# Kernel tuning notes

Hardware: AMD Instinct MI355X
Metric: run time of the kernel (lower is better)

## Reference

```python
import jax, jax.numpy as jnp
import numpy as np

MAX_INT = 1e4  # sentinel used by the original (transitions into START / out of STOP forbidden)
VOCAB, E, H, T, B, S = 50257, 512, 1024, 50, 8, 512  # T = tagset_size + 2


def _lstm_scan(x, h0, c0, Wih, Whh, b):
    # x: [time, batch, E] (time axis is the ORIGINAL batch dim, faithful to the
    # torch code which feeds [B,S,E] into a batch_first=False LSTM)
    def step(carry, xt):
        h, c = carry
        g = xt @ Wih.T + h @ Whh.T + b
        i, f, gg, o = jnp.split(g, 4, axis=-1)  # torch gate order i,f,g,o
        c = jax.nn.sigmoid(f) * c + jax.nn.sigmoid(i) * jnp.tanh(gg)
        h = jax.nn.sigmoid(o) * jnp.tanh(c)
        return (h, c), h
    _, hs = jax.lax.scan(step, (h0, c0), x)
    return hs


def setup_inputs() -> dict:
    key = jax.random.key(0)
    k = jax.random.split(key, 14)
    Hd = H // 2
    X = jax.random.randint(k[0], (B, S), 0, VOCAB)
    Y = jax.random.randint(k[1], (B, S), 0, T - 2)  # real tags only (no start/stop)
    h0 = jax.random.normal(k[2], (2, S, Hd), jnp.float32)
    c0 = jax.random.normal(k[3], (2, S, Hd), jnp.float32)
    emb_table = jax.random.normal(k[4], (VOCAB, E), jnp.float32) * 0.02
    Wih_f = jax.random.normal(k[5], (4 * Hd, E), jnp.float32) * 0.05
    Whh_f = jax.random.normal(k[6], (4 * Hd, Hd), jnp.float32) * 0.05
    b_f = jnp.zeros((4 * Hd,), jnp.float32)
    Wih_b = jax.random.normal(k[7], (4 * Hd, E), jnp.float32) * 0.05
    Whh_b = jax.random.normal(k[8], (4 * Hd, Hd), jnp.float32) * 0.05
    b_b = jnp.zeros((4 * Hd,), jnp.float32)
    fc_W = jax.random.normal(k[9], (T, H), jnp.float32) * 0.05
    fc_b = jnp.zeros((T,), jnp.float32)
    tr = jax.random.normal(k[10], (T, T), jnp.float32)
    transitions = tr.at[-2, :].set(-MAX_INT).at[:, -1].set(-MAX_INT)
    return {"X": X, "Y": Y, "h0": h0, "c0": c0, "emb_table": emb_table,
            "Wih_f": Wih_f, "Whh_f": Whh_f, "b_f": b_f,
            "Wih_b": Wih_b, "Whh_b": Whh_b, "b_b": b_b,
            "fc_W": fc_W, "fc_b": fc_b, "transitions": transitions}


def reference(X, Y, h0, c0, emb_table, Wih_f, Whh_f, b_f, Wih_b, Whh_b, b_b, fc_W, fc_b, transitions):
    emb = emb_table[X]                                   # [B,S,E]
    # BiLSTM: torch sees axis0 as time (faithful quirk), hidden batch == S
    hf = _lstm_scan(emb, h0[0], c0[0], Wih_f, Whh_f, b_f)
    hb = _lstm_scan(emb[::-1], h0[1], c0[1], Wih_b, Whh_b, b_b)[::-1]
    lstm_out = jnp.concatenate([hf, hb], axis=-1)        # [B,S,H]
    feats = lstm_out @ fc_W.T + fc_b                     # [B,S,T]
    nB, Tt = X.shape[0], transitions.shape[0]
    # CRF forward algorithm (log partition), vectorized over tags
    init = jnp.full((nB, Tt), -MAX_INT, feats.dtype).at[:, -2].set(0.0)
    def crf_step(fv, feat):                              # fv [B,T], feat [B,T]
        nv = fv[:, None, :] + transitions[None, :, :] + feat[:, :, None]  # [B,next,prev]
        return jax.nn.logsumexp(nv, axis=2), None
    fv, _ = jax.lax.scan(crf_step, init, jnp.swapaxes(feats, 0, 1))
    forward_score = jax.nn.logsumexp(fv + transitions[-1][None, :], axis=1).sum()
    # gold path score
    start = jnp.full((nB, 1), Tt - 2, dtype=Y.dtype)
    tags = jnp.concatenate([start, Y], axis=1)           # [B,S+1]
    trans_sc = transitions[tags[:, 1:], tags[:, :-1]].sum()
    emit_sc = jnp.take_along_axis(feats, tags[:, 1:, None], axis=2)[..., 0].sum()
    gold_score = trans_sc + emit_sc + transitions[-1, tags[:, -1]].sum()
    score = forward_score - gold_score
    return score, Y
```

## Files before the change

kernel.cpp:

```cpp
#include <hip/hip_runtime.h>
#include <hip/hip_bf16.h>

typedef __attribute__((ext_vector_type(4))) float f32x4;
typedef __attribute__((ext_vector_type(8))) short short8;

#define LN2F 0.69314718055994531f

__device__ __forceinline__ unsigned short f2b(float x){
  union{float f;unsigned u;}v; v.f=x;
  unsigned r = v.u + 0x7fffu + ((v.u>>16)&1u);
  return (unsigned short)(r>>16);
}
__device__ __forceinline__ float b2f(unsigned short h){
  union{unsigned u;float f;}v; v.u = ((unsigned)h)<<16; return v.f;
}
__device__ __forceinline__ float sigm(float x){ return 1.f/(1.f+__expf(-x)); }
__device__ __forceinline__ float tanh_(float x){ float t=__expf(2.f*x); return 1.f - 2.f/(t+1.f); }

__global__ __launch_bounds__(256) void prep_kernel(
  const int* __restrict__ X, const int* __restrict__ Y,
  const float* __restrict__ h0, const float* __restrict__ c0,
  const float* __restrict__ emb,
  const float* __restrict__ WihF, const float* __restrict__ WihB,
  const float* __restrict__ WhhFf, const float* __restrict__ WhhBf,
  const float* __restrict__ fcWf, const float* __restrict__ trans,
  unsigned short* __restrict__ Abf, unsigned short* __restrict__ Wcat,
  unsigned short* __restrict__ WhhF, unsigned short* __restrict__ WhhB,
  unsigned short* __restrict__ hbufs, float* __restrict__ cbuf,
  unsigned short* __restrict__ fcW, unsigned short* __restrict__ Ebf,
  float* __restrict__ out)
{
  const int tid = blockIdx.x*256 + threadIdx.x;
  const int nth = gridDim.x*256;
  for(int i=tid;i<524288;i+=nth){
    int r = i>>7, q = i&127;
    float4 v = ((const float4*)(emb + (size_t)X[r]*512))[q];
    ushort4 o; o.x=f2b(v.x); o.y=f2b(v.y); o.z=f2b(v.z); o.w=f2b(v.w);
    ((ushort4*)Abf)[i] = o;
  }
  for(int i=tid;i<524288;i+=nth){
    int r = i>>7, q = i&127;
    const float* src = (r<2048) ? (WihF + (size_t)r*512) : (WihB + (size_t)(r-2048)*512);
    float4 v = ((const float4*)src)[q];
    ushort4 o; o.x=f2b(v.x); o.y=f2b(v.y); o.z=f2b(v.z); o.w=f2b(v.w);
    ((ushort4*)Wcat)[i] = o;
  }
  for(int i=tid;i<262144;i+=nth){
    float4 v = ((const float4*)WhhFf)[i];
    ushort4 o; o.x=f2b(v.x); o.y=f2b(v.y); o.z=f2b(v.z); o.w=f2b(v.w);
    ((ushort4*)WhhF)[i] = o;
  }
  for(int i=tid;i<262144;i+=nth){
    float4 v = ((const float4*)WhhBf)[i];
    ushort4 o; o.x=f2b(v.x); o.y=f2b(v.y); o.z=f2b(v.z); o.w=f2b(v.w);
    ((ushort4*)WhhB)[i] = o;
  }
  for(int i=tid;i<131072;i+=nth){
    int d = i>>16, rest = i&65535;
    float4 v = ((const float4*)h0)[i];
    ushort4 o; o.x=f2b(v.x); o.y=f2b(v.y); o.z=f2b(v.z); o.w=f2b(v.w);
    ((ushort4*)hbufs)[(size_t)(d*2)*65536 + rest] = o;
  }
  for(int i=tid;i<131072;i+=nth) ((float4*)cbuf)[i] = ((const float4*)c0)[i];
  for(int i=tid;i<16384;i+=nth){
    int n = i>>8, q = i&255;
    float4 v;
    if (n<50) v = ((const float4*)(fcWf + (size_t)n*1024))[q];
    else { v.x=0.f; v.y=0.f; v.z=0.f; v.w=0.f; }
    ushort4 o; o.x=f2b(v.x); o.y=f2b(v.y); o.z=f2b(v.z); o.w=f2b(v.w);
    ((ushort4*)fcW)[i] = o;
  }
  for(int i=tid;i<4096;i+=nth){
    int n = i>>6, p = i&63;
    float v = (n<50 && p<50) ? __expf(trans[n*50+p]) : 0.f;
    Ebf[i] = f2b(v);
  }
  for(int i=tid;i<4096;i+=nth) out[1+i] = (float)Y[i];
}

__global__ __launch_bounds__(256) void gemm1_kernel(const unsigned short* __restrict__ A,
                                                    const unsigned short* __restrict__ B,
                                                    unsigned short* __restrict__ C){
  __shared__ __align__(16) unsigned short As[128*40];
  __shared__ __align__(16) unsigned short Bs[128*40];
  const int t = threadIdx.x, w = t>>6, l = t&63;
  const int m0 = blockIdx.x<<7, n0 = blockIdx.y<<7;
  const int wr = (w>>1)<<6, wc = (w&1)<<6;
  const int srow = t>>2, scol = (t&3)<<3;
  const int fr = l&15, fk = (l>>4)<<3;
  f32x4 acc[4][4];
  #pragma unroll
  for(int i=0;i<4;i++)
    #pragma unroll
    for(int j=0;j<4;j++) acc[i][j]=(f32x4)0.f;
  const unsigned short* Ab = A + (size_t)m0*512;
  const unsigned short* Bb = B + (size_t)n0*512;
  uint4 pa0 = *(const uint4*)(Ab + srow*512 + scol);
  uint4 pa1 = *(const uint4*)(Ab + (64+srow)*512 + scol);
  uint4 pb0 = *(const uint4*)(Bb + srow*512 + scol);
  uint4 pb1 = *(const uint4*)(Bb + (64+srow)*512 + scol);
  for(int kt=0; kt<16; ++kt){
    __syncthreads();
    *(uint4*)&As[srow*40 + scol] = pa0;
    *(uint4*)&As[(64+srow)*40 + scol] = pa1;
    *(uint4*)&Bs[srow*40 + scol] = pb0;
    *(uint4*)&Bs[(64+srow)*40 + scol] = pb1;
    __syncthreads();
    if (kt<15){
      int kc = (kt+1)*32 + scol;
      pa0 = *(const uint4*)(Ab + srow*512 + kc);
      pa1 = *(const uint4*)(Ab + (64+srow)*512 + kc);
      pb0 = *(const uint4*)(Bb + srow*512 + kc);
      pb1 = *(const uint4*)(Bb + (64+srow)*512 + kc);
    }
    short8 af[4], bf[4];
    #pragma unroll
    for(int mi=0;mi<4;mi++) af[mi] = *(const short8*)&As[(wr+mi*16+fr)*40 + fk];
    #pragma unroll
    for(int ni=0;ni<4;ni++) bf[ni] = *(const short8*)&Bs[(wc+ni*16+fr)*40 + fk];
    #pragma unroll
    for(int mi=0;mi<4;mi++)
      #pragma unroll
      for(int ni=0;ni<4;ni++)
        acc[mi][ni] = __builtin_amdgcn_mfma_f32_16x16x32_bf16(af[mi], bf[ni], acc[mi][ni], 0,0,0);
  }
  #pragma unroll
  for(int mi=0;mi<4;mi++)
    #pragma unroll
    for(int ni=0;ni<4;ni++)
      #pragma unroll
      for(int j=0;j<4;j++){
        int row = m0 + wr + mi*16 + ((l>>4)<<2) + j;
        int col = n0 + wc + ni*16 + fr;
        C[(size_t)row*4096 + col] = f2b(acc[mi][ni][j]);
      }
}

__global__ __launch_bounds__(256) void lstm_step_kernel(
  unsigned short* __restrict__ hbufs, float* __restrict__ cbuf,
  unsigned short* __restrict__ hall, const unsigned short* __restrict__ Gin,
  const unsigned short* __restrict__ WhhF_, const unsigned short* __restrict__ WhhB_,
  const float* __restrict__ bF, const float* __restrict__ bB, int t)
{
  __shared__ __align__(16) unsigned short Ah[128*40];
  __shared__ __align__(16) unsigned short Bw[64*40];
  const int d = blockIdx.z;
  const int m0 = blockIdx.x<<7;
  const int u0 = blockIdx.y<<4;
  const int tin = d ? (7-t) : t;
  const int par = t&1;
  const unsigned short* hprev = hbufs + (size_t)(d*2+par)*262144;
  unsigned short* hnext = hbufs + (size_t)(d*2+(par^1))*262144;
  const unsigned short* W = d ? WhhB_ : WhhF_;
  const float* bias = d ? bB : bF;
  const int tx = threadIdx.x, w = tx>>6, l = tx&63;
  const int srow = tx>>2, scol = (tx&3)<<3;
  const int bc = tx>>2;
  const int bn = ((bc>>4)<<9) + u0 + (bc&15);
  const int fr = l&15, fk = (l>>4)<<3;
  f32x4 acc[2][4];
  #pragma unroll
  for(int i=0;i<2;i++)
    #pragma unroll
    for(int j=0;j<4;j++) acc[i][j]=(f32x4)0.f;
  uint4 pa0 = *(const uint4*)(hprev + (size_t)(m0+srow)*512 + scol);
  uint4 pa1 = *(const uint4*)(hprev + (size_t)(m0+64+srow)*512 + scol);
  uint4 pb0 = *(const uint4*)(W + (size_t)bn*512 + scol);
  for(int kt=0; kt<16; ++kt){
    __syncthreads();
    *(uint4*)&Ah[srow*40+scol] = pa0;
    *(uint4*)&Ah[(64+srow)*40+scol] = pa1;
    *(uint4*)&Bw[bc*40+scol] = pb0;
    __syncthreads();
    if(kt<15){
      int kc = (kt+1)*32 + scol;
      pa0 = *(const uint4*)(hprev + (size_t)(m0+srow)*512 + kc);
      pa1 = *(const uint4*)(hprev + (size_t)(m0+64+srow)*512 + kc);
      pb0 = *(const uint4*)(W + (size_t)bn*512 + kc);
    }
    short8 af[2], bf[4];
    #pragma unroll
    for(int mi=0;mi<2;mi++) af[mi] = *(const short8*)&Ah[(w*32+mi*16+fr)*40 + fk];
    #pragma unroll
    for(int g=0;g<4;g++)   bf[g]  = *(const short8*)&Bw[(g*16+fr)*40 + fk];
    #pragma unroll
    for(int mi=0;mi<2;mi++)
      #pragma unroll
      for(int g=0;g<4;g++)
        acc[mi][g] = __builtin_amdgcn_mfma_f32_16x16x32_bf16(af[mi], bf[g], acc[mi][g], 0,0,0);
  }
  #pragma unroll
  for(int mi=0;mi<2;mi++)
    #pragma unroll
    for(int j=0;j<4;j++){
      int rs = m0 + w*32 + mi*16 + ((l>>4)<<2) + j;
      int u  = u0 + fr;
      size_t grow = (size_t)(tin*512 + rs)*4096 + (size_t)d*2048;
      float p0 = acc[mi][0][j] + b2f(Gin[grow +    0 + u]) + bias[   0+u];
      float p1 = acc[mi][1][j] + b2f(Gin[grow +  512 + u]) + bias[ 512+u];
      float p2 = acc[mi][2][j] + b2f(Gin[grow + 1024 + u]) + bias[1024+u];
      float p3 = acc[mi][3][j] + b2f(Gin[grow + 1536 + u]) + bias[1536+u];
      size_t ci = (size_t)d*262144 + (size_t)rs*512 + u;
      float c = sigm(p1)*cbuf[ci] + sigm(p0)*tanh_(p2);
      cbuf[ci] = c;
      float h = sigm(p3)*tanh_(c);
      hnext[(size_t)rs*512+u] = f2b(h);
      hall[(size_t)(tin*512+rs)*1024 + (size_t)d*512 + u] = f2b(h);
    }
}

__global__ __launch_bounds__(256) void fc_kernel(const unsigned short* __restrict__ hA,
    const unsigned short* __restrict__ Wf, const float* __restrict__ fcb,
    float* __restrict__ feats){
  __shared__ __align__(16) unsigned short As[128*40];
  __shared__ __align__(16) unsigned short Bs[64*40];
  const int tx = threadIdx.x, w = tx>>6, l = tx&63;
  const int m0 = blockIdx.x<<7;
  const int srow = tx>>2, scol = (tx&3)<<3;
  const int fr=l&15, fk=(l>>4)<<3;
  f32x4 acc[2][4];
  #pragma unroll
  for(int i=0;i<2;i++)
    #pragma unroll
    for(int j=0;j<4;j++) acc[i][j]=(f32x4)0.f;
  uint4 pa0 = *(const uint4*)(hA + (size_t)(m0+srow)*1024 + scol);
  uint4 pa1 = *(const uint4*)(hA + (size_t)(m0+64+srow)*1024 + scol);
  uint4 pb0 = *(const uint4*)(Wf + (size_t)srow*1024 + scol);
  for(int kt=0; kt<32; ++kt){
    __syncthreads();
    *(uint4*)&As[srow*40+scol] = pa0;
    *(uint4*)&As[(64+srow)*40+scol] = pa1;
    *(uint4*)&Bs[srow*40+scol] = pb0;
    __syncthreads();
    if(kt<31){
      int kc = (kt+1)*32 + scol;
      pa0 = *(const uint4*)(hA + (size_t)(m0+srow)*1024 + kc);
      pa1 = *(const uint4*)(hA + (size_t)(m0+64+srow)*1024 + kc);
      pb0 = *(const uint4*)(Wf + (size_t)srow*1024 + kc);
    }
    short8 af[2], bf[4];
    #pragma unroll
    for(int mi=0;mi<2;mi++) af[mi] = *(const short8*)&As[(w*32+mi*16+fr)*40 + fk];
    #pragma unroll
    for(int ni=0;ni<4;ni++) bf[ni] = *(const short8*)&Bs[(ni*16+fr)*40 + fk];
    #pragma unroll
    for(int mi=0;mi<2;mi++)
      #pragma unroll
      for(int ni=0;ni<4;ni++)
        acc[mi][ni] = __builtin_amdgcn_mfma_f32_16x16x32_bf16(af[mi], bf[ni], acc[mi][ni], 0,0,0);
  }
  #pragma unroll
  for(int mi=0;mi<2;mi++)
    #pragma unroll
    for(int ni=0;ni<4;ni++)
      #pragma unroll
      for(int j=0;j<4;j++){
        int rs = m0 + w*32 + mi*16 + ((l>>4)<<2) + j;
        int n  = ni*16 + fr;
        feats[(size_t)rs*64+n] = acc[mi][ni][j] + (n<50 ? fcb[n] : 0.f);
      }
}

__global__ __launch_bounds__(64) void crf_group_kernel(
    const float* __restrict__ feats, const unsigned short* __restrict__ Ebf,
    float* __restrict__ Wout, int* __restrict__ kexp)
{
  __shared__ __align__(16) unsigned short PT[64*72];
  __shared__ float fe[8*64];
  const int g = blockIdx.x, b = blockIdx.y;
  const int l = threadIdx.x;
  const int lj = l & 15, q = l >> 4;
  const float* fb = feats + (size_t)(b*512 + g*8)*64;
  #pragma unroll
  for(int j=0;j<8;j++) fe[j*64 + l] = fb[j*64 + l];
  short8 afE[4][2];
  #pragma unroll
  for(int i=0;i<4;i++)
    #pragma unroll
    for(int h=0;h<2;h++)
      afE[i][h] = *(const short8*)(Ebf + (i*16+lj)*64 + h*32 + q*8);
  {
    uint4 erow[8];
    #pragma unroll
    for(int i=0;i<8;i++) erow[i] = *(const uint4*)(Ebf + l*64 + i*8);
    float ef0 = __expf(fe[l]);
    const unsigned* e32 = (const unsigned*)erow;
    #pragma unroll
    for(int m=0;m<64;m++){
      unsigned short eb = (unsigned short)(e32[m>>1] >> ((m&1)*16));
      PT[m*72 + l] = f2b(b2f(eb) * ef0);
    }
  }
  float sc_lag = 1.f;
  int exprev = 0, kblk = 0;
  #pragma unroll
  for(int k=1;k<8;k++){
    kblk += exprev;
    float ev[4][4];
    #pragma unroll
    for(int i=0;i<4;i++)
      #pragma unroll
      for(int r=0;r<4;r++)
        ev[i][r] = __expf(fe[k*64 + i*16 + q*4 + r]) * sc_lag;
    short8 bfP[4][2];
    #pragma unroll
    for(int j=0;j<4;j++)
      #pragma unroll
      for(int h=0;h<2;h++)
        bfP[j][h] = *(const short8*)&PT[(j*16+lj)*72 + h*32 + q*8];
    f32x4 acc[4][4];
    #pragma unroll
    for(int i=0;i<4;i++)
      #pragma unroll
      for(int j=0;j<4;j++) acc[i][j] = (f32x4)0.f;
    #pragma unroll
    for(int h=0;h<2;h++)
      #pragma unroll
      for(int i=0;i<4;i++)
        #pragma unroll
        for(int j=0;j<4;j++)
          acc[i][j] = __builtin_amdgcn_mfma_f32_16x16x32_bf16(afE[i][h], bfP[j][h], acc[i][j], 0,0,0);
    float mx = 1e-30f;
    float* Wo = Wout + (size_t)(b*64 + g)*4096;
    #pragma unroll
    for(int i=0;i<4;i++)
      #pragma unroll
      for(int j=0;j<4;j++){
        float v0 = acc[i][j][0]*ev[i][0];
        float v1 = acc[i][j][1]*ev[i][1];
        float v2 = acc[i][j][2]*ev[i][2];
        float v3 = acc[i][j][3]*ev[i][3];
        mx = fmaxf(fmaxf(mx, fmaxf(v0,v1)), fmaxf(v2,v3));
        int base = (j*16+lj)*72 + i*16 + q*4;
        *(unsigned*)&PT[base]   = (unsigned)f2b(v0) | ((unsigned)f2b(v1)<<16);
        *(unsigned*)&PT[base+2] = (unsigned)f2b(v2) | ((unsigned)f2b(v3)<<16);
        if(k==7){
          int n = i*16 + q*4, m = j*16 + lj;
          Wo[(size_t)(n+0)*64 + m] = v0;
          Wo[(size_t)(n+1)*64 + m] = v1;
          Wo[(size_t)(n+2)*64 + m] = v2;
          Wo[(size_t)(n+3)*64 + m] = v3;
        }
      }
    #pragma unroll
    for(int off=1; off<64; off<<=1) mx = fmaxf(mx, __shfl_xor(mx, off));
    int ex = ((__builtin_bit_cast(int, mx) >> 23) & 0xff) - 127;
    ex = ex < -120 ? -120 : (ex > 120 ? 120 : ex);
    sc_lag = __builtin_bit_cast(float, (unsigned)((127-ex)<<23));
    exprev = ex;
  }
  if(l==0) kexp[b*64 + g] = kblk;
}

__global__ __launch_bounds__(64) void crf_seq_kernel(const float* __restrict__ W,
    const int* __restrict__ kexp, const float* __restrict__ trans,
    float* __restrict__ scores){
  __shared__ __align__(16) float sh[64];
  const int b = blockIdx.x, l = threadIdx.x;
  const float* Wb = W + (size_t)b*262144;
  float kl = (float)kexp[b*64 + l];
  #pragma unroll
  for(int off=32;off;off>>=1) kl += __shfl_down(kl, off);
  float G = (l==48) ? 1.f : 0.f;
  float sc = 1.f, Mrun = 0.f;
  int exprev = 0;
  float4 curA[16], curB[16];
  #pragma unroll
  for(int i=0;i<16;i++) curA[i] = ((const float4*)(Wb + (size_t)l*64))[i];

#define SEQ_STEP(CUR, NXT, GI) {                                            \
    sh[l] = G;                                                              \
    const float* wn = Wb + (size_t)(((GI)+1)&63)*4096 + (size_t)l*64;       \
    _Pragma("unroll")                                                       \
    for(int i=0;i<16;i++) NXT[i] = ((const float4*)wn)[i];                  \
    float4 gq[16];                                                          \
    _Pragma("unroll")                                                       \
    for(int i=0;i<16;i++) gq[i] = ((const float4*)sh)[i];                   \
    float a0=0.f,a1=0.f,a2=0.f,a3=0.f;                                      \
    _Pragma("unroll")                                                       \
    for(int i=0;i<16;i++){                                                  \
      a0 = fmaf(CUR[i].x, gq[i].x, a0);                                     \
      a1 = fmaf(CUR[i].y, gq[i].y, a1);                                     \
      a2 = fmaf(CUR[i].z, gq[i].z, a2);                                     \
      a3 = fmaf(CUR[i].w, gq[i].w, a3);                                     \
    }                                                                       \
    float S = (a0+a1)+(a2+a3);                                              \
    Mrun += (float)exprev;                                                  \
    G = S * sc;                                                             \
    float Sp = __builtin_bit_cast(float, __builtin_amdgcn_readfirstlane(    \
                 __builtin_bit_cast(int, fmaxf(S, 1e-35f))));               \
    int ex = ((__builtin_bit_cast(int, Sp) >> 23) & 0xff) - 127;            \
    ex = ex < -120 ? -120 : (ex > 120 ? 120 : ex);                          \
    sc = __builtin_bit_cast(float, (unsigned)((127-ex)<<23));               \
    exprev = ex;                                                            \
  }

  for(int g=0; g<64; g+=2){
    SEQ_STEP(curA, curB, g)
    SEQ_STEP(curB, curA, g+1)
  }
#undef SEQ_STEP
  float u = (l<50) ? __expf(trans[49*50+l]) : 0.f;
  float val = G * u;
  #pragma unroll
  for(int off=32;off;off>>=1) val += __shfl_down(val, off);
  if(l==0) scores[b] = logf(fmaxf(val,1e-35f)) + (Mrun + kl)*LN2F;
}

__global__ __launch_bounds__(256) void final_kernel(const int* __restrict__ Y,
   const float* __restrict__ trans, const float* __restrict__ feats,
   const float* __restrict__ scores, float* __restrict__ out){
  const int tx = threadIdx.x;
  float acc = 0.f;
  for(int i=tx; i<4096; i+=256){
    int s = i & 511;
    int y = Y[i];
    int prev = s ? Y[i-1] : 48;
    acc += trans[y*50+prev] + feats[(size_t)i*64+y];
    if (s==511) acc += trans[49*50+y];
  }
  #pragma unroll
  for(int off=32; off; off>>=1) acc += __shfl_down(acc, off);
  __shared__ float red[4];
  if((tx&63)==0) red[tx>>6] = acc;
  __syncthreads();
  if(tx==0){
    float gold = red[0]+red[1]+red[2]+red[3];
    float fwd = 0.f;
    #pragma unroll
    for(int b=0;b<8;b++) fwd += scores[b];
    out[0] = fwd - gold;
  }
}

extern "C" void kernel_launch(void* const* d_in, const int* in_sizes, int n_in,
                              void* d_out, int out_size, void* d_ws, size_t ws_size,
                              hipStream_t stream) {
  (void)in_sizes; (void)n_in; (void)out_size; (void)ws_size;
  const int*   X     = (const int*)d_in[0];
  const int*   Y     = (const int*)d_in[1];
  const float* h0    = (const float*)d_in[2];
  const float* c0    = (const float*)d_in[3];
  const float* emb   = (const float*)d_in[4];
  const float* WihF  = (const float*)d_in[5];
  const float* WhhFf = (const float*)d_in[6];
  const float* bF    = (const float*)d_in[7];
  const float* WihB  = (const float*)d_in[8];
  const float* WhhBf = (const float*)d_in[9];
  const float* bB    = (const float*)d_in[10];
  const float* fcWf  = (const float*)d_in[11];
  const float* fcb   = (const float*)d_in[12];
  const float* trans = (const float*)d_in[13];
  float* out = (float*)d_out;
  char* ws = (char*)d_ws;

  unsigned short* Abf   = (unsigned short*)(ws + 0);
  unsigned short* Wcat  = (unsigned short*)(ws + 4194304);
  unsigned short* WhhF  = (unsigned short*)(ws + 8388608);
  unsigned short* WhhB  = (unsigned short*)(ws + 10485760);
  unsigned short* Gin   = (unsigned short*)(ws + 12582912);
  float*          Wgrp  = (float*)(ws + 12582912);
  int*            kexp  = (int*)(ws + 20971520);
  unsigned short* hbufs = (unsigned short*)(ws + 46137344);
  float*          cbuf  = (float*)(ws + 48234496);
  unsigned short* hall  = (unsigned short*)(ws + 50331648);
  unsigned short* fcW   = (unsigned short*)(ws + 58720256);
  float*          feats = (float*)(ws + 58851328);
  unsigned short* Ebf   = (unsigned short*)(ws + 59900160);
  float*          scores= (float*)(ws + 59913472);

  hipLaunchKernelGGL(prep_kernel, dim3(1024), dim3(256), 0, stream,
      X, Y, h0, c0, emb, WihF, WihB, WhhFf, WhhBf, fcWf, trans,
      Abf, Wcat, WhhF, WhhB, hbufs, cbuf, fcW, Ebf, out);
  hipLaunchKernelGGL(gemm1_kernel, dim3(32,32), dim3(256), 0, stream, Abf, Wcat, Gin);
  for(int t=0;t<8;t++)
    hipLaunchKernelGGL(lstm_step_kernel, dim3(4,32,2), dim3(256), 0, stream,
        hbufs, cbuf, hall, Gin, WhhF, WhhB, bF, bB, t);
  hipLaunchKernelGGL(fc_kernel, dim3(32), dim3(256), 0, stream, hall, fcW, fcb, feats);
  hipLaunchKernelGGL(crf_group_kernel, dim3(64,8), dim3(64), 0, stream, feats, Ebf, Wgrp, kexp);
  hipLaunchKernelGGL(crf_seq_kernel, dim3(8), dim3(64), 0, stream, Wgrp, kexp, trans, scores);
  hipLaunchKernelGGL(final_kernel, dim3(1), dim3(256), 0, stream, Y, trans, feats, scores, out);
}
```

Measured before the change: 234.3 us.

## Fuse LSTM timesteps into persistent cooperative kernel and widen CRF groups

```diff
diff --git a/kernel.cpp b/kernel.cpp
--- a/kernel.cpp
+++ b/kernel.cpp
@@ -1,5 +1,8 @@
 #include <hip/hip_runtime.h>
 #include <hip/hip_bf16.h>
+#include <hip/hip_cooperative_groups.h>
+
+namespace cg = cooperative_groups;
 
 typedef __attribute__((ext_vector_type(4))) float f32x4;
 typedef __attribute__((ext_vector_type(8))) short short8;
@@ -136,77 +139,86 @@
       }
 }
 
-__global__ __launch_bounds__(256) void lstm_step_kernel(
+__global__ __launch_bounds__(256, 1) void lstm_coop_kernel(
   unsigned short* __restrict__ hbufs, float* __restrict__ cbuf,
   unsigned short* __restrict__ hall, const unsigned short* __restrict__ Gin,
   const unsigned short* __restrict__ WhhF_, const unsigned short* __restrict__ WhhB_,
-  const float* __restrict__ bF, const float* __restrict__ bB, int t)
+  const float* __restrict__ bF, const float* __restrict__ bB)
 {
-  __shared__ __align__(16) unsigned short Ah[128*40];
-  __shared__ __align__(16) unsigned short Bw[64*40];
-  const int d = blockIdx.z;
-  const int m0 = blockIdx.x<<7;
-  const int u0 = blockIdx.y<<4;
-  const int tin = d ? (7-t) : t;
-  const int par = t&1;
-  const unsigned short* hprev = hbufs + (size_t)(d*2+par)*262144;
-  unsigned short* hnext = hbufs + (size_t)(d*2+(par^1))*262144;
+  __shared__ __align__(16) unsigned short WL[16*64*32];
+  cg::grid_group grid = cg::this_grid();
+  const int bid = blockIdx.x;
+  const int d  = bid >> 7;
+  const int m0 = ((bid >> 5) & 3) << 7;
+  const int u0 = (bid & 31) << 4;
   const unsigned short* W = d ? WhhB_ : WhhF_;
   const float* bias = d ? bB : bF;
   const int tx = threadIdx.x, w = tx>>6, l = tx&63;
-  const int srow = tx>>2, scol = (tx&3)<<3;
-  const int bc = tx>>2;
-  const int bn = ((bc>>4)<<9) + u0 + (bc&15);
-  const int fr = l&15, fk = (l>>4)<<3;
-  f32x4 acc[2][4];
-  #pragma unroll
-  for(int i=0;i<2;i++)
-    #pragma unroll
-    for(int j=0;j<4;j++) acc[i][j]=(f32x4)0.f;
-  uint4 pa0 = *(const uint4*)(hprev + (size_t)(m0+srow)*512 + scol);
-  uint4 pa1 = *(const uint4*)(hprev + (size_t)(m0+64+srow)*512 + scol);
-  uint4 pb0 = *(const uint4*)(W + (size_t)bn*512 + scol);
-  for(int kt=0; kt<16; ++kt){
-    __syncthreads();
-    *(uint4*)&Ah[srow*40+scol] = pa0;
-    *(uint4*)&Ah[(64+srow)*40+scol] = pa1;
-    *(uint4*)&Bw[bc*40+scol] = pb0;
-    __syncthreads();
-    if(kt<15){
-      int kc = (kt+1)*32 + scol;
-      pa0 = *(const uint4*)(hprev + (size_t)(m0+srow)*512 + kc);
-      pa1 = *(const uint4*)(hprev + (size_t)(m0+64+srow)*512 + kc);
-      pb0 = *(const uint4*)(W + (size_t)bn*512 + kc);
+  const int fr = l&15, q = l>>4;
+  {
+    const int row = tx >> 2, qq = tx & 3;
+    const int g = row >> 4, ul = row & 15;
+    const int grow = (g<<9) + u0 + ul;
+    #pragma unroll
+    for(int kt=0;kt<16;kt++){
+      uint4 v = *(const uint4*)(W + (size_t)grow*512 + kt*32 + qq*8);
+      *(uint4*)((char*)WL + (((kt*4 + g)*64) + (qq*16 + ul))*16) = v;
     }
-    short8 af[2], bf[4];
-    #pragma unroll
-    for(int mi=0;mi<2;mi++) af[mi] = *(const short8*)&Ah[(w*32+mi*16+fr)*40 + fk];
-    #pragma unroll
-    for(int g=0;g<4;g++)   bf[g]  = *(const short8*)&Bw[(g*16+fr)*40 + fk];
+  }
+  __syncthreads();
+  for(int t=0;t<8;t++){
+    const int tin = d ? (7-t) : t;
+    const int par = t&1;
+    const unsigned short* hprev = hbufs + (size_t)(d*2+par)*262144;
+    unsigned short* hnext = hbufs + (size_t)(d*2+(par^1))*262144;
+    f32x4 acc[2][4];
+    #pragma unroll
+    for(int i=0;i<2;i++)
+      #pragma unroll
+      for(int j=0;j<4;j++) acc[i][j]=(f32x4)0.f;
+    const unsigned short* arow0 = hprev + (size_t)(m0 + w*32 + fr)*512 + q*8;
+    const unsigned short* arow1 = arow0 + (size_t)16*512;
+    uint4 af0 = *(const uint4*)arow0;
+    uint4 af1 = *(const uint4*)arow1;
+    for(int kt=0; kt<16; ++kt){
+      uint4 nf0 = af0, nf1 = af1;
+      if(kt<15){
+        nf0 = *(const uint4*)(arow0 + (kt+1)*32);
+        nf1 = *(const uint4*)(arow1 + (kt+1)*32);
+      }
+      short8 a0 = __builtin_bit_cast(short8, af0);
+      short8 a1 = __builtin_bit_cast(short8, af1);
+      short8 bf[4];
+      #pragma unroll
+      for(int g=0;g<4;g++)
+        bf[g] = *(const short8*)((char*)WL + (((kt*4 + g)*64) + l)*16);
+      #pragma unroll
+      for(int g=0;g<4;g++){
+        acc[0][g] = __builtin_amdgcn_mfma_f32_16x16x32_bf16(a0, bf[g], acc[0][g], 0,0,0);
+        acc[1][g] = __builtin_amdgcn_mfma_f32_16x16x32_bf16(a1, bf[g], acc[1][g], 0,0,0);
+      }
+      af0 = nf0; af1 = nf1;
+    }
     #pragma unroll
     for(int mi=0;mi<2;mi++)
       #pragma unroll
-      for(int g=0;g<4;g++)
-        acc[mi][g] = __builtin_amdgcn_mfma_f32_16x16x32_bf16(af[mi], bf[g], acc[mi][g], 0,0,0);
-  }
-  #pragma unroll
-  for(int mi=0;mi<2;mi++)
-    #pragma unroll
-    for(int j=0;j<4;j++){
-      int rs = m0 + w*32 + mi*16 + ((l>>4)<<2) + j;
-      int u  = u0 + fr;
-      size_t grow = (size_t)(tin*512 + rs)*4096 + (size_t)d*2048;
-      float p0 = acc[mi][0][j] + b2f(Gin[grow +    0 + u]) + bias[   0+u];
-      float p1 = acc[mi][1][j] + b2f(Gin[grow +  512 + u]) + bias[ 512+u];
-      float p2 = acc[mi][2][j] + b2f(Gin[grow + 1024 + u]) + bias[1024+u];
-      float p3 = acc[mi][3][j] + b2f(Gin[grow + 1536 + u]) + bias[1536+u];
-      size_t ci = (size_t)d*262144 + (size_t)rs*512 + u;
-      float c = sigm(p1)*cbuf[ci] + sigm(p0)*tanh_(p2);
-      cbuf[ci] = c;
-      float h = sigm(p3)*tanh_(c);
-      hnext[(size_t)rs*512+u] = f2b(h);
-      hall[(size_t)(tin*512+rs)*1024 + (size_t)d*512 + u] = f2b(h);
-    }
+      for(int j=0;j<4;j++){
+        int rs = m0 + w*32 + mi*16 + (q<<2) + j;
+        int u  = u0 + fr;
+        size_t grow = (size_t)(tin*512 + rs)*4096 + (size_t)d*2048;
+        float p0 = acc[mi][0][j] + b2f(Gin[grow +    0 + u]) + bias[   0+u];
+        float p1 = acc[mi][1][j] + b2f(Gin[grow +  512 + u]) + bias[ 512+u];
+        float p2 = acc[mi][2][j] + b2f(Gin[grow + 1024 + u]) + bias[1024+u];
+        float p3 = acc[mi][3][j] + b2f(Gin[grow + 1536 + u]) + bias[1536+u];
+        size_t ci = (size_t)d*262144 + (size_t)rs*512 + u;
+        float c = sigm(p1)*cbuf[ci] + sigm(p0)*tanh_(p2);
+        cbuf[ci] = c;
+        float h = sigm(p3)*tanh_(c);
+        hnext[(size_t)rs*512+u] = f2b(h);
+        hall[(size_t)(tin*512+rs)*1024 + (size_t)d*512 + u] = f2b(h);
+      }
+    if(t<7) grid.sync();
+  }
 }
 
 __global__ __launch_bounds__(256) void fc_kernel(const unsigned short* __restrict__ hA,
@@ -266,13 +278,13 @@
     float* __restrict__ Wout, int* __restrict__ kexp)
 {
   __shared__ __align__(16) unsigned short PT[64*72];
-  __shared__ float fe[8*64];
+  __shared__ float fe[16*64];
   const int g = blockIdx.x, b = blockIdx.y;
   const int l = threadIdx.x;
   const int lj = l & 15, q = l >> 4;
-  const float* fb = feats + (size_t)(b*512 + g*8)*64;
-  #pragma unroll
-  for(int j=0;j<8;j++) fe[j*64 + l] = fb[j*64 + l];
+  const float* fb = feats + (size_t)(b*512 + g*16)*64;
+  #pragma unroll
+  for(int j=0;j<16;j++) fe[j*64 + l] = fb[j*64 + l];
   short8 afE[4][2];
   #pragma unroll
   for(int i=0;i<4;i++)
@@ -294,7 +306,7 @@
   float sc_lag = 1.f;
   int exprev = 0, kblk = 0;
   #pragma unroll
-  for(int k=1;k<8;k++){
+  for(int k=1;k<16;k++){
     kblk += exprev;
     float ev[4][4];
     #pragma unroll
@@ -321,7 +333,7 @@
         for(int j=0;j<4;j++)
           acc[i][j] = __builtin_amdgcn_mfma_f32_16x16x32_bf16(afE[i][h], bfP[j][h], acc[i][j], 0,0,0);
     float mx = 1e-30f;
-    float* Wo = Wout + (size_t)(b*64 + g)*4096;
+    float* Wo = Wout + (size_t)(b*32 + g)*4096;
     #pragma unroll
     for(int i=0;i<4;i++)
       #pragma unroll
@@ -334,7 +346,7 @@
         int base = (j*16+lj)*72 + i*16 + q*4;
         *(unsigned*)&PT[base]   = (unsigned)f2b(v0) | ((unsigned)f2b(v1)<<16);
         *(unsigned*)&PT[base+2] = (unsigned)f2b(v2) | ((unsigned)f2b(v3)<<16);
-        if(k==7){
+        if(k==15){
           int n = i*16 + q*4, m = j*16 + lj;
           Wo[(size_t)(n+0)*64 + m] = v0;
           Wo[(size_t)(n+1)*64 + m] = v1;
@@ -349,7 +361,7 @@
     sc_lag = __builtin_bit_cast(float, (unsigned)((127-ex)<<23));
     exprev = ex;
   }
-  if(l==0) kexp[b*64 + g] = kblk;
+  if(l==0) kexp[b*32 + g] = kblk;
 }
 
 __global__ __launch_bounds__(64) void crf_seq_kernel(const float* __restrict__ W,
@@ -357,8 +369,8 @@
     float* __restrict__ scores){
   __shared__ __align__(16) float sh[64];
   const int b = blockIdx.x, l = threadIdx.x;
-  const float* Wb = W + (size_t)b*262144;
-  float kl = (float)kexp[b*64 + l];
+  const float* Wb = W + (size_t)b*131072;
+  float kl = (l<32) ? (float)kexp[b*32 + l] : 0.f;
   #pragma unroll
   for(int off=32;off;off>>=1) kl += __shfl_down(kl, off);
   float G = (l==48) ? 1.f : 0.f;
@@ -370,7 +382,7 @@
 
 #define SEQ_STEP(CUR, NXT, GI) {                                            \
     sh[l] = G;                                                              \
-    const float* wn = Wb + (size_t)(((GI)+1)&63)*4096 + (size_t)l*64;       \
+    const float* wn = Wb + (size_t)(((GI)+1)&31)*4096 + (size_t)l*64;       \
     _Pragma("unroll")                                                       \
     for(int i=0;i<16;i++) NXT[i] = ((const float4*)wn)[i];                  \
     float4 gq[16];                                                          \
@@ -395,7 +407,7 @@
     exprev = ex;                                                            \
   }
 
-  for(int g=0; g<64; g+=2){
+  for(int g=0; g<32; g+=2){
     SEQ_STEP(curA, curB, g)
     SEQ_STEP(curB, curA, g+1)
   }
@@ -473,11 +485,17 @@
       X, Y, h0, c0, emb, WihF, WihB, WhhFf, WhhBf, fcWf, trans,
       Abf, Wcat, WhhF, WhhB, hbufs, cbuf, fcW, Ebf, out);
   hipLaunchKernelGGL(gemm1_kernel, dim3(32,32), dim3(256), 0, stream, Abf, Wcat, Gin);
-  for(int t=0;t<8;t++)
-    hipLaunchKernelGGL(lstm_step_kernel, dim3(4,32,2), dim3(256), 0, stream,
-        hbufs, cbuf, hall, Gin, WhhF, WhhB, bF, bB, t);
+  {
+    const unsigned short* GinC = Gin;
+    const unsigned short* WhhFc = WhhF;
+    const unsigned short* WhhBc = WhhB;
+    void* args[] = { (void*)&hbufs, (void*)&cbuf, (void*)&hall, (void*)&GinC,
+                     (void*)&WhhFc, (void*)&WhhBc, (void*)&bF, (void*)&bB };
+    hipLaunchCooperativeKernel((const void*)lstm_coop_kernel, dim3(256), dim3(256),
+                               args, 0, stream);
+  }
   hipLaunchKernelGGL(fc_kernel, dim3(32), dim3(256), 0, stream, hall, fcW, fcb, feats);
-  hipLaunchKernelGGL(crf_group_kernel, dim3(64,8), dim3(64), 0, stream, feats, Ebf, Wgrp, kexp);
+  hipLaunchKernelGGL(crf_group_kernel, dim3(32,8), dim3(64), 0, stream, feats, Ebf, Wgrp, kexp);
   hipLaunchKernelGGL(crf_seq_kernel, dim3(8), dim3(64), 0, stream, Wgrp, kexp, trans, scores);
   hipLaunchKernelGGL(final_kernel, dim3(1), dim3(256), 0, stream, Y, trans, feats, scores, out);
 }
```

Result: slower. 441.6 us (+88.5%).
